# Kernel tuning notes

Hardware: AMD Instinct MI355X
Metric: run time of the kernel (lower is better)

Reference implementation:

```python
import jax, jax.numpy as jnp
import numpy as np
from jax import lax

B, C, H, W = 8, 64, 96, 96
OC = 64
KH = KW = 3
DG = 1
STRIDE = 1
PAD = 1
DIL = 1


def setup_inputs() -> dict:
    key = jax.random.key(0)
    k1, k2, k3, k4, k5 = jax.random.split(key, 5)
    x = jax.random.normal(k1, (B, C, H, W), jnp.float32)
    off_ch = DG * 3 * KH * KW
    # small random offset/mask conv params (the original inits them to zero,
    # which would make offsets degenerate; small values exercise the sampler)
    w_off = jax.random.normal(k2, (off_ch, C, KH, KW), jnp.float32) * 0.01
    b_off = jax.random.normal(k3, (off_ch,), jnp.float32) * 0.01
    stdv = 1.0 / float(np.sqrt(C * KH * KW))
    weight = jax.random.uniform(k4, (OC, C, KH, KW), jnp.float32, -stdv, stdv)
    bias = jax.random.uniform(k5, (OC,), jnp.float32, -stdv, stdv)
    return {"x": x, "w_off": w_off, "b_off": b_off, "weight": weight, "bias": bias}


def _deform_conv(x, w_off, b_off, weight, bias):
    Bt, Ct, Ht, Wt = x.shape
    K = KH * KW
    # standard conv producing offsets + mask logits
    om = lax.conv_general_dilated(
        x, w_off, (STRIDE, STRIDE), ((PAD, PAD), (PAD, PAD)),
        rhs_dilation=(DIL, DIL), dimension_numbers=("NCHW", "OIHW", "NCHW"),
    ) + b_off[None, :, None, None]
    o1, o2, m = jnp.split(om, 3, axis=1)  # each [B, DG*K, Ho, Wo]
    Ho, Wo = o1.shape[2], o1.shape[3]
    mask = jax.nn.sigmoid(m).reshape(Bt, DG, 1, K, Ho, Wo)
    off_y = o1.reshape(Bt, DG, K, Ho, Wo)
    off_x = o2.reshape(Bt, DG, K, Ho, Wo)
    # base sampling grid: p = out_pos*stride - pad + k*dilation + offset
    kk = jnp.arange(K)
    base_y = (kk // KW)[:, None] * DIL + (jnp.arange(Ho) * STRIDE - PAD)[None, :]  # [K, Ho]
    base_x = (kk % KW)[:, None] * DIL + (jnp.arange(Wo) * STRIDE - PAD)[None, :]   # [K, Wo]
    py = off_y + base_y[None, None, :, :, None].astype(x.dtype)  # [B, DG, K, Ho, Wo]
    px = off_x + base_x[None, None, :, None, :].astype(x.dtype)
    y0 = jnp.floor(py)
    x0 = jnp.floor(px)
    ly = py - y0
    lx = px - x0
    Cg = Ct // DG
    xg = x.reshape(Bt, DG, Cg, Ht * Wt)

    def gath(xf, idx):  # xf [Cg, H*W], idx [K*Ho*Wo]
        return jnp.take(xf, idx, axis=1)

    gather = jax.vmap(jax.vmap(gath))  # over B, DG

    sampled = jnp.zeros((Bt, DG, Cg, K, Ho, Wo), x.dtype)
    for dy, dx, wgt in ((0, 0, (1 - ly) * (1 - lx)), (0, 1, (1 - ly) * lx),
                        (1, 0, ly * (1 - lx)), (1, 1, ly * lx)):
        yy = y0 + dy
        xx = x0 + dx
        valid = (yy >= 0) & (yy < Ht) & (xx >= 0) & (xx < Wt)
        yi = jnp.clip(yy, 0, Ht - 1).astype(jnp.int32)
        xi = jnp.clip(xx, 0, Wt - 1).astype(jnp.int32)
        idx = (yi * Wt + xi).reshape(Bt, DG, K * Ho * Wo)
        v = gather(xg, idx).reshape(Bt, DG, Cg, K, Ho, Wo)
        sampled = sampled + v * (wgt * valid)[:, :, None]
    sampled = sampled * mask  # modulated
    wr = weight.reshape(OC, DG, Cg, K)
    out = jnp.einsum("bgckhw,ogck->bohw", sampled, wr) + bias[None, :, None, None]
    return out


def reference(x, w_off, b_off, weight, bias):
    return _deform_conv(x, w_off, b_off, weight, bias)
```

## Files before the change

kernel.cpp:

```cpp
#include <hip/hip_runtime.h>
#include <math.h>

#define Bn 8
#define Cn 64
#define Hn 96
#define Wn 96
#define HWn (Hn*Wn)
#define OCn 64
#define Kn 9
#define OFFCn 27
#define NPIX (Bn*HWn)
#define PGRPS (NPIX/64)

#define WPK1_N 15552
#define WPK2M_SHORTS 131072
#define WS_DWORDS (45*NPIX + WPK1_N + WPK2M_SHORTS/2)
#define WS_BYTES  ((size_t)WS_DWORDS*4)

typedef __attribute__((ext_vector_type(8))) short short8v;
typedef __attribute__((ext_vector_type(4))) float f32x4;

static __device__ __forceinline__ unsigned short bf16_rne(float f) {
    unsigned int u = __float_as_uint(f);
    return (unsigned short)((u + 0x7FFFu + ((u >> 16) & 1u)) >> 16);
}
static __device__ __forceinline__ float bf16_back(unsigned short h) {
    return __uint_as_float(((unsigned int)h) << 16);
}

__global__ __launch_bounds__(256) void dcn_wprep(
    const float* __restrict__ w_off,
    const float* __restrict__ weight,
    float* __restrict__ wpk1,
    short* __restrict__ wpk2m)
{
    const int g = blockIdx.x * 256 + threadIdx.x;
    if (g < WPK1_N) {
        const int c_all = g / 243;
        const int och   = (g % 243) / 9;
        const int ki    = g % 9;
        wpk1[g] = w_off[(och * 64 + c_all) * 9 + ki];
    }
    if (g < WPK2M_SHORTS / 8) {
        const int lane = g & 63;
        const int oct  = (g >> 6) & 3;
        const int c    = g >> 8;
        const int oc   = oct * 16 + (lane & 15);
        const float* wsrc = weight + (oc * 64 + c) * 9;
        short8v v;
#pragma unroll
        for (int j = 0; j < 8; ++j) {
            const int s = ((lane >> 4) & 3) * 8 + j;
            float f = 0.0f;
            if (s <= 8)                f = wsrc[s];
            else if (s >= 16 && s <= 24) f = wsrc[s - 16];
            v[j] = (short)bf16_rne(f);
        }
        ((short8v*)wpk2m)[g] = v;
    }
}

__global__ __launch_bounds__(256, 2) void dcn_k1(
    const float* __restrict__ x,
    const float* __restrict__ wpk1,
    const float* __restrict__ b_off,
    float* __restrict__ pwbuf,
    int*   __restrict__ abuf)
{
    __shared__ float lds[4 * 64 * OFFCn];

    const int tid  = threadIdx.x;
    const int lane = tid & 63;
    const int wv   = tid >> 6;
    const int cbase = __builtin_amdgcn_readfirstlane(wv * 16);

    const int p  = blockIdx.x * 64 + lane;
    const int b  = p / HWn;
    const int hw = p % HWn;
    const int ho = hw / Wn;
    const int wo = hw % Wn;

    const float* xb = x + b * (Cn * HWn);

    int   toff[Kn];
    float tval[Kn];
#pragma unroll
    for (int ki = 0; ki < Kn; ++ki) {
        const int yy = ho + ki / 3 - 1, xx = wo + ki % 3 - 1;
        const bool v = (yy >= 0) && (yy < Hn) && (xx >= 0) && (xx < Wn);
        toff[ki] = min(max(yy, 0), Hn - 1) * Wn + min(max(xx, 0), Wn - 1);
        tval[ki] = v ? 1.0f : 0.0f;
    }

    float om[OFFCn];
#pragma unroll
    for (int j = 0; j < OFFCn; ++j) om[j] = 0.0f;

    const float* wstream = wpk1 + cbase * 243;
    for (int ci = 0; ci < 16; ++ci) {
        const float* xc = xb + (cbase + ci) * HWn;
        float xk[Kn];
#pragma unroll
        for (int ki = 0; ki < Kn; ++ki)
            xk[ki] = xc[toff[ki]] * tval[ki];

        const float* wc = wstream + ci * 243;
#pragma unroll
        for (int och = 0; och < OFFCn; ++och) {
            const float* wp = wc + och * 9;
            float a = om[och];
#pragma unroll
            for (int ki = 0; ki < Kn; ++ki)
                a = fmaf(xk[ki], wp[ki], a);
            om[och] = a;
        }
    }

#pragma unroll
    for (int j = 0; j < OFFCn; ++j)
        lds[(wv * 64 + lane) * OFFCn + j] = om[j];
    __syncthreads();
#pragma unroll
    for (int j = 0; j < OFFCn; ++j) {
        float a = b_off[j];
#pragma unroll
        for (int ww = 0; ww < 4; ++ww)
            a += lds[(ww * 64 + lane) * OFFCn + j];
        om[j] = a;
    }

    float pw0[Kn], pw1[Kn], pw2[Kn], pw3[Kn];
    int   pav[Kn];
#pragma unroll
    for (int ki = 0; ki < Kn; ++ki) {
        const float py = om[ki]      + (float)(ki / 3 + ho - 1);
        const float px = om[Kn + ki] + (float)(ki % 3 + wo - 1);
        const float m  = 1.0f / (1.0f + __expf(-om[2 * Kn + ki]));

        const float y0f = floorf(py), x0f = floorf(px);
        const float ly = py - y0f, lx = px - x0f;
        const int iy0 = (int)y0f, ix0 = (int)x0f;
        const int iy1 = iy0 + 1,  ix1 = ix0 + 1;

        const float vy0 = (iy0 >= 0 && iy0 < Hn) ? 1.0f : 0.0f;
        const float vy1 = (iy1 >= 0 && iy1 < Hn) ? 1.0f : 0.0f;
        const float vx0 = (ix0 >= 0 && ix0 < Wn) ? 1.0f : 0.0f;
        const float vx1 = (ix1 >= 0 && ix1 < Wn) ? 1.0f : 0.0f;

        const int iy0c = min(max(iy0, 0), Hn - 1);
        const int iy1c = min(max(iy1, 0), Hn - 1);
        const int ix0c = min(max(ix0, 0), Wn - 1);
        const int ix1c = min(max(ix1, 0), Wn - 1);

        pw0[ki] = m * (1.0f - ly) * (1.0f - lx) * vy0 * vx0;
        pw1[ki] = m * (1.0f - ly) * lx          * vy0 * vx1;
        pw2[ki] = m * ly          * (1.0f - lx) * vy1 * vx0;
        pw3[ki] = m * ly          * lx          * vy1 * vx1;
        const int pa  = iy0c * Wn + ix0c;
        const int dx  = ix1c - ix0c;
        const int dyw = (iy1c - iy0c) * Wn;
        pav[ki] = pa | (dx << 16) | (dyw << 17);
    }

    if (wv == 0) {
#pragma unroll
        for (int ki = 0; ki < Kn; ++ki) pwbuf[(0 * Kn + ki) * NPIX + p] = pw0[ki];
#pragma unroll
        for (int ki = 0; ki < Kn; ++ki) abuf[ki * NPIX + p] = pav[ki];
    } else if (wv == 1) {
#pragma unroll
        for (int ki = 0; ki < Kn; ++ki) pwbuf[(1 * Kn + ki) * NPIX + p] = pw1[ki];
    } else if (wv == 2) {
#pragma unroll
        for (int ki = 0; ki < Kn; ++ki) pwbuf[(2 * Kn + ki) * NPIX + p] = pw2[ki];
    } else {
#pragma unroll
        for (int ki = 0; ki < Kn; ++ki) pwbuf[(3 * Kn + ki) * NPIX + p] = pw3[ki];
    }
}

__global__ __launch_bounds__(256, 2) void dcn_k2(
    const float* __restrict__ x,
    const short* __restrict__ wpk2m,
    const float* __restrict__ bias,
    const float* __restrict__ pwbuf,
    const int*   __restrict__ abuf,
    float* __restrict__ out)
{
    __shared__ short smp[32 * 64 * 8];

    const int tid  = threadIdx.x;
    const int lane = tid & 63;
    const int wv   = tid >> 6;

    const int p0  = blockIdx.x * 64;
    const int b   = p0 / HWn;
    const int hwb = p0 % HWn;
    const int p   = p0 + lane;

    const float* xb = x + b * (Cn * HWn);

    float pw0[Kn], pw1[Kn], pw2[Kn], pw3[Kn];
    int   pav[Kn];
#pragma unroll
    for (int ki = 0; ki < Kn; ++ki) pw0[ki] = pwbuf[(0 * Kn + ki) * NPIX + p];
#pragma unroll
    for (int ki = 0; ki < Kn; ++ki) pw1[ki] = pwbuf[(1 * Kn + ki) * NPIX + p];
#pragma unroll
    for (int ki = 0; ki < Kn; ++ki) pw2[ki] = pwbuf[(2 * Kn + ki) * NPIX + p];
#pragma unroll
    for (int ki = 0; ki < Kn; ++ki) pw3[ki] = pwbuf[(3 * Kn + ki) * NPIX + p];
#pragma unroll
    for (int ki = 0; ki < Kn; ++ki) pav[ki] = abuf[ki * NPIX + p];

    f32x4 acc[4];
#pragma unroll
    for (int oct = 0; oct < 4; ++oct) acc[oct] = (f32x4){0.f, 0.f, 0.f, 0.f};

    const short8v* afrags = (const short8v*)wpk2m;

    for (int chunk = 0; chunk < 8; ++chunk) {
#pragma unroll
        for (int cc = 0; cc < 2; ++cc) {
            const int cl = (wv << 1) | cc;
            const float* xc = xb + (chunk * 8 + cl) * HWn;
            unsigned short hi[Kn], lo[Kn];
#pragma unroll
            for (int ki = 0; ki < Kn; ++ki) {
                const int av  = pav[ki];
                const int pa  = av & 0xFFFF;
                const int dx  = (av >> 16) & 1;
                const int dyw = av >> 17;
                const float* bp = xc + pa;
                const float v = pw0[ki] * bp[0] + pw1[ki] * bp[dx]
                              + pw2[ki] * bp[dyw] + pw3[ki] * bp[dyw + dx];
                hi[ki] = bf16_rne(v);
                lo[ki] = bf16_rne(v - bf16_back(hi[ki]));
            }
            short8v h0, h1, l0, l1;
#pragma unroll
            for (int j = 0; j < 8; ++j) { h0[j] = (short)hi[j]; l0[j] = (short)lo[j]; }
            h1 = (short8v){(short)hi[8], 0, 0, 0, 0, 0, 0, 0};
            l1 = (short8v){(short)lo[8], 0, 0, 0, 0, 0, 0, 0};
            const int r0 = cl * 4;
            *(short8v*)&smp[((r0 + 0) * 64 + lane) * 8] = h0;
            *(short8v*)&smp[((r0 + 1) * 64 + lane) * 8] = h1;
            *(short8v*)&smp[((r0 + 2) * 64 + lane) * 8] = l0;
            *(short8v*)&smp[((r0 + 3) * 64 + lane) * 8] = l1;
        }
        __syncthreads();

#pragma unroll
        for (int ks = 0; ks < 8; ++ks) {
            const short8v bfrag = *(const short8v*)
                &smp[((ks * 4 + (lane >> 4)) * 64 + wv * 16 + (lane & 15)) * 8];
#pragma unroll
            for (int oct = 0; oct < 4; ++oct) {
                const short8v afrag =
                    afrags[(((chunk * 8 + ks) * 4) + oct) * 64 + lane];
                acc[oct] = __builtin_amdgcn_mfma_f32_16x16x32_bf16(
                    afrag, bfrag, acc[oct], 0, 0, 0);
            }
        }
        __syncthreads();
    }

    const int pxl = wv * 16 + (lane & 15);
    float* ob = out + b * (OCn * HWn) + hwb + pxl;
#pragma unroll
    for (int oct = 0; oct < 4; ++oct) {
#pragma unroll
        for (int r = 0; r < 4; ++r) {
            const int oc = oct * 16 + ((lane >> 4) & 3) * 4 + r;
            ob[oc * HWn] = acc[oct][r] + bias[oc];
        }
    }
}

__global__ __launch_bounds__(64) void dcn_r1(
    const float* __restrict__ x,
    const float* __restrict__ w_off,
    const float* __restrict__ b_off,
    const float* __restrict__ weight,
    const float* __restrict__ bias,
    float* __restrict__ out)
{
    const int p  = blockIdx.x * 64 + threadIdx.x;
    const int b  = p / HWn;
    const int hw = p % HWn;
    const int ho = hw / Wn;
    const int wo = hw % Wn;
    const float* xb = x + b * (Cn * HWn);

    float om[OFFCn];
#pragma unroll
    for (int j = 0; j < OFFCn; ++j) om[j] = b_off[j];

    int   toff[Kn];
    float tval[Kn];
#pragma unroll
    for (int ki = 0; ki < Kn; ++ki) {
        const int yy = ho + ki / 3 - 1, xx = wo + ki % 3 - 1;
        const bool v = (yy >= 0) && (yy < Hn) && (xx >= 0) && (xx < Wn);
        toff[ki] = min(max(yy, 0), Hn - 1) * Wn + min(max(xx, 0), Wn - 1);
        tval[ki] = v ? 1.0f : 0.0f;
    }
    for (int c = 0; c < Cn; ++c) {
        const float* xc = xb + c * HWn;
        float xk[Kn];
#pragma unroll
        for (int ki = 0; ki < Kn; ++ki) xk[ki] = xc[toff[ki]] * tval[ki];
        const float* wc = w_off + c * Kn;
#pragma unroll
        for (int och = 0; och < OFFCn; ++och) {
            const float* wp = wc + och * (Cn * Kn);
            float a = om[och];
#pragma unroll
            for (int ki = 0; ki < Kn; ++ki) a = fmaf(xk[ki], wp[ki], a);
            om[och] = a;
        }
    }
    float pw0[Kn], pw1[Kn], pw2[Kn], pw3[Kn];
    int   pa[Kn], pdx[Kn], pdyw[Kn];
#pragma unroll
    for (int ki = 0; ki < Kn; ++ki) {
        const float py = om[ki]      + (float)(ki / 3 + ho - 1);
        const float px = om[Kn + ki] + (float)(ki % 3 + wo - 1);
        const float m  = 1.0f / (1.0f + __expf(-om[2 * Kn + ki]));
        const float y0f = floorf(py), x0f = floorf(px);
        const float ly = py - y0f, lx = px - x0f;
        const int iy0 = (int)y0f, ix0 = (int)x0f;
        const int iy1 = iy0 + 1,  ix1 = ix0 + 1;
        const float vy0 = (iy0 >= 0 && iy0 < Hn) ? 1.0f : 0.0f;
        const float vy1 = (iy1 >= 0 && iy1 < Hn) ? 1.0f : 0.0f;
        const float vx0 = (ix0 >= 0 && ix0 < Wn) ? 1.0f : 0.0f;
        const float vx1 = (ix1 >= 0 && ix1 < Wn) ? 1.0f : 0.0f;
        const int iy0c = min(max(iy0, 0), Hn - 1);
        const int iy1c = min(max(iy1, 0), Hn - 1);
        const int ix0c = min(max(ix0, 0), Wn - 1);
        const int ix1c = min(max(ix1, 0), Wn - 1);
        pw0[ki] = m * (1.0f - ly) * (1.0f - lx) * vy0 * vx0;
        pw1[ki] = m * (1.0f - ly) * lx          * vy0 * vx1;
        pw2[ki] = m * ly          * (1.0f - lx) * vy1 * vx0;
        pw3[ki] = m * ly          * lx          * vy1 * vx1;
        pa[ki]   = iy0c * Wn + ix0c;
        pdx[ki]  = ix1c - ix0c;
        pdyw[ki] = (iy1c - iy0c) * Wn;
    }
    float acc[OCn];
#pragma unroll
    for (int oc = 0; oc < OCn; ++oc) acc[oc] = bias[oc];
    for (int c = 0; c < Cn; ++c) {
        const float* xc = xb + c * HWn;
        float s[Kn];
#pragma unroll
        for (int ki = 0; ki < Kn; ++ki) {
            const float* bp = xc + pa[ki];
            s[ki] = pw0[ki] * bp[0] + pw1[ki] * bp[pdx[ki]]
                  + pw2[ki] * bp[pdyw[ki]] + pw3[ki] * bp[pdyw[ki] + pdx[ki]];
        }
        const float* wc = weight + c * Kn;
#pragma unroll
        for (int oc = 0; oc < OCn; ++oc) {
            const float* wp = wc + oc * (Cn * Kn);
            float a = acc[oc];
#pragma unroll
            for (int ki = 0; ki < Kn; ++ki) a = fmaf(s[ki], wp[ki], a);
            acc[oc] = a;
        }
    }
    float* ob = out + b * (OCn * HWn) + hw;
#pragma unroll
    for (int oc = 0; oc < OCn; ++oc) ob[oc * HWn] = acc[oc];
}

extern "C" void kernel_launch(void* const* d_in, const int* in_sizes, int n_in,
                              void* d_out, int out_size, void* d_ws, size_t ws_size,
                              hipStream_t stream) {
    const float* x      = (const float*)d_in[0];
    const float* w_off  = (const float*)d_in[1];
    const float* b_off  = (const float*)d_in[2];
    const float* weight = (const float*)d_in[3];
    const float* bias   = (const float*)d_in[4];
    float* out = (float*)d_out;

    if (ws_size >= WS_BYTES) {
        float* pwbuf = (float*)d_ws;
        int*   abuf  = (int*)((float*)d_ws + 36 * NPIX);
        float* wpk1  = (float*)d_ws + 45 * NPIX;
        short* wpk2m = (short*)(wpk1 + WPK1_N);
        hipLaunchKernelGGL(dcn_wprep, dim3(64), dim3(256), 0, stream,
                           w_off, weight, wpk1, wpk2m);
        hipLaunchKernelGGL(dcn_k1, dim3(PGRPS), dim3(256), 0, stream,
                           x, wpk1, b_off, pwbuf, abuf);
        hipLaunchKernelGGL(dcn_k2, dim3(PGRPS), dim3(256), 0, stream,
                           x, wpk2m, bias, pwbuf, abuf, out);
    } else {
        hipLaunchKernelGGL(dcn_r1, dim3(NPIX / 64), dim3(64), 0, stream,
                           x, w_off, b_off, weight, bias, out);
    }
}
```

Baseline: 261.5 us.

## Fuse offset-conv and deformable sampling kernels into one kernel

```diff
diff --git a/kernel.cpp b/kernel.cpp
--- a/kernel.cpp
+++ b/kernel.cpp
@@ -14,7 +14,7 @@
 
 #define WPK1_N 15552
 #define WPK2M_SHORTS 131072
-#define WS_DWORDS (45*NPIX + WPK1_N + WPK2M_SHORTS/2)
+#define WS_DWORDS (WPK1_N + WPK2M_SHORTS/2)
 #define WS_BYTES  ((size_t)WS_DWORDS*4)
 
 typedef __attribute__((ext_vector_type(8))) short short8v;
@@ -52,7 +52,7 @@
         for (int j = 0; j < 8; ++j) {
             const int s = ((lane >> 4) & 3) * 8 + j;
             float f = 0.0f;
-            if (s <= 8)                f = wsrc[s];
+            if (s <= 8)                  f = wsrc[s];
             else if (s >= 16 && s <= 24) f = wsrc[s - 16];
             v[j] = (short)bf16_rne(f);
         }
@@ -60,73 +60,79 @@
     }
 }
 
-__global__ __launch_bounds__(256, 2) void dcn_k1(
+__global__ __launch_bounds__(256, 2) void dcn_fused(
     const float* __restrict__ x,
     const float* __restrict__ wpk1,
     const float* __restrict__ b_off,
-    float* __restrict__ pwbuf,
-    int*   __restrict__ abuf)
+    const short* __restrict__ wpk2m,
+    const float* __restrict__ bias,
+    float* __restrict__ out)
 {
-    __shared__ float lds[4 * 64 * OFFCn];
+    __shared__ short smp[32 * 64 * 8];
+    float* lds1 = (float*)smp;
 
     const int tid  = threadIdx.x;
     const int lane = tid & 63;
     const int wv   = tid >> 6;
     const int cbase = __builtin_amdgcn_readfirstlane(wv * 16);
 
-    const int p  = blockIdx.x * 64 + lane;
-    const int b  = p / HWn;
-    const int hw = p % HWn;
-    const int ho = hw / Wn;
-    const int wo = hw % Wn;
+    const int p0  = blockIdx.x * 64;
+    const int b   = p0 / HWn;
+    const int hwb = p0 % HWn;
+    const int p   = p0 + lane;
+    const int hw  = p % HWn;
+    const int ho  = hw / Wn;
+    const int wo  = hw % Wn;
 
     const float* xb = x + b * (Cn * HWn);
 
-    int   toff[Kn];
-    float tval[Kn];
-#pragma unroll
-    for (int ki = 0; ki < Kn; ++ki) {
-        const int yy = ho + ki / 3 - 1, xx = wo + ki % 3 - 1;
-        const bool v = (yy >= 0) && (yy < Hn) && (xx >= 0) && (xx < Wn);
-        toff[ki] = min(max(yy, 0), Hn - 1) * Wn + min(max(xx, 0), Wn - 1);
-        tval[ki] = v ? 1.0f : 0.0f;
-    }
-
     float om[OFFCn];
-#pragma unroll
-    for (int j = 0; j < OFFCn; ++j) om[j] = 0.0f;
-
-    const float* wstream = wpk1 + cbase * 243;
-    for (int ci = 0; ci < 16; ++ci) {
-        const float* xc = xb + (cbase + ci) * HWn;
-        float xk[Kn];
-#pragma unroll
-        for (int ki = 0; ki < Kn; ++ki)
-            xk[ki] = xc[toff[ki]] * tval[ki];
-
-        const float* wc = wstream + ci * 243;
-#pragma unroll
-        for (int och = 0; och < OFFCn; ++och) {
-            const float* wp = wc + och * 9;
-            float a = om[och];
+    {
+        int   toff[Kn];
+        float tval[Kn];
+#pragma unroll
+        for (int ki = 0; ki < Kn; ++ki) {
+            const int yy = ho + ki / 3 - 1, xx = wo + ki % 3 - 1;
+            const bool v = (yy >= 0) && (yy < Hn) && (xx >= 0) && (xx < Wn);
+            toff[ki] = min(max(yy, 0), Hn - 1) * Wn + min(max(xx, 0), Wn - 1);
+            tval[ki] = v ? 1.0f : 0.0f;
+        }
+
+#pragma unroll
+        for (int j = 0; j < OFFCn; ++j) om[j] = 0.0f;
+
+        const float* wstream = wpk1 + cbase * 243;
+        for (int ci = 0; ci < 16; ++ci) {
+            const float* xc = xb + (cbase + ci) * HWn;
+            float xk[Kn];
 #pragma unroll
             for (int ki = 0; ki < Kn; ++ki)
-                a = fmaf(xk[ki], wp[ki], a);
-            om[och] = a;
-        }
-    }
-
-#pragma unroll
-    for (int j = 0; j < OFFCn; ++j)
-        lds[(wv * 64 + lane) * OFFCn + j] = om[j];
-    __syncthreads();
-#pragma unroll
-    for (int j = 0; j < OFFCn; ++j) {
-        float a = b_off[j];
-#pragma unroll
-        for (int ww = 0; ww < 4; ++ww)
-            a += lds[(ww * 64 + lane) * OFFCn + j];
-        om[j] = a;
+                xk[ki] = xc[toff[ki]] * tval[ki];
+
+            const float* wc = wstream + ci * 243;
+#pragma unroll
+            for (int och = 0; och < OFFCn; ++och) {
+                const float* wp = wc + och * 9;
+                float a = om[och];
+#pragma unroll
+                for (int ki = 0; ki < Kn; ++ki)
+                    a = fmaf(xk[ki], wp[ki], a);
+                om[och] = a;
+            }
+        }
+
+#pragma unroll
+        for (int j = 0; j < OFFCn; ++j)
+            lds1[(wv * 64 + lane) * OFFCn + j] = om[j];
+        __syncthreads();
+#pragma unroll
+        for (int j = 0; j < OFFCn; ++j) {
+            float a = b_off[j];
+#pragma unroll
+            for (int ww = 0; ww < 4; ++ww)
+                a += lds1[(ww * 64 + lane) * OFFCn + j];
+            om[j] = a;
+        }
     }
 
     float pw0[Kn], pw1[Kn], pw2[Kn], pw3[Kn];
@@ -161,57 +167,7 @@
         const int dyw = (iy1c - iy0c) * Wn;
         pav[ki] = pa | (dx << 16) | (dyw << 17);
     }
-
-    if (wv == 0) {
-#pragma unroll
-        for (int ki = 0; ki < Kn; ++ki) pwbuf[(0 * Kn + ki) * NPIX + p] = pw0[ki];
-#pragma unroll
-        for (int ki = 0; ki < Kn; ++ki) abuf[ki * NPIX + p] = pav[ki];
-    } else if (wv == 1) {
-#pragma unroll
-        for (int ki = 0; ki < Kn; ++ki) pwbuf[(1 * Kn + ki) * NPIX + p] = pw1[ki];
-    } else if (wv == 2) {
-#pragma unroll
-        for (int ki = 0; ki < Kn; ++ki) pwbuf[(2 * Kn + ki) * NPIX + p] = pw2[ki];
-    } else {
-#pragma unroll
-        for (int ki = 0; ki < Kn; ++ki) pwbuf[(3 * Kn + ki) * NPIX + p] = pw3[ki];
-    }
-}
-
-__global__ __launch_bounds__(256, 2) void dcn_k2(
-    const float* __restrict__ x,
-    const short* __restrict__ wpk2m,
-    const float* __restrict__ bias,
-    const float* __restrict__ pwbuf,
-    const int*   __restrict__ abuf,
-    float* __restrict__ out)
-{
-    __shared__ short smp[32 * 64 * 8];
-
-    const int tid  = threadIdx.x;
-    const int lane = tid & 63;
-    const int wv   = tid >> 6;
-
-    const int p0  = blockIdx.x * 64;
-    const int b   = p0 / HWn;
-    const int hwb = p0 % HWn;
-    const int p   = p0 + lane;
-
-    const float* xb = x + b * (Cn * HWn);
-
-    float pw0[Kn], pw1[Kn], pw2[Kn], pw3[Kn];
-    int   pav[Kn];
-#pragma unroll
-    for (int ki = 0; ki < Kn; ++ki) pw0[ki] = pwbuf[(0 * Kn + ki) * NPIX + p];
-#pragma unroll
-    for (int ki = 0; ki < Kn; ++ki) pw1[ki] = pwbuf[(1 * Kn + ki) * NPIX + p];
-#pragma unroll
-    for (int ki = 0; ki < Kn; ++ki) pw2[ki] = pwbuf[(2 * Kn + ki) * NPIX + p];
-#pragma unroll
-    for (int ki = 0; ki < Kn; ++ki) pw3[ki] = pwbuf[(3 * Kn + ki) * NPIX + p];
-#pragma unroll
-    for (int ki = 0; ki < Kn; ++ki) pav[ki] = abuf[ki * NPIX + p];
+    __syncthreads();
 
     f32x4 acc[4];
 #pragma unroll
@@ -385,16 +341,12 @@
     float* out = (float*)d_out;
 
     if (ws_size >= WS_BYTES) {
-        float* pwbuf = (float*)d_ws;
-        int*   abuf  = (int*)((float*)d_ws + 36 * NPIX);
-        float* wpk1  = (float*)d_ws + 45 * NPIX;
+        float* wpk1  = (float*)d_ws;
         short* wpk2m = (short*)(wpk1 + WPK1_N);
         hipLaunchKernelGGL(dcn_wprep, dim3(64), dim3(256), 0, stream,
                            w_off, weight, wpk1, wpk2m);
-        hipLaunchKernelGGL(dcn_k1, dim3(PGRPS), dim3(256), 0, stream,
-                           x, wpk1, b_off, pwbuf, abuf);
-        hipLaunchKernelGGL(dcn_k2, dim3(PGRPS), dim3(256), 0, stream,
-                           x, wpk2m, bias, pwbuf, abuf, out);
+        hipLaunchKernelGGL(dcn_fused, dim3(PGRPS), dim3(256), 0, stream,
+                           x, wpk1, b_off, wpk2m, bias, out);
     } else {
         hipLaunchKernelGGL(dcn_r1, dim3(NPIX / 64), dim3(64), 0, stream,
                            x, w_off, b_off, weight, bias, out);
```

Measured after the change: 272.2 us. +4.1%, slower.
